# Kernel tuning notes

Hardware: AMD Instinct MI355X
Metric: run time of the kernel (lower is better)

Reference implementation:

```python
import jax, jax.numpy as jnp
import numpy as np

V = 32000   # shared src/trg vocab size
E = 128     # EMB_DIM
H = 256     # HID_DIM
B = 32      # batch
S = 64      # src len
T = 64      # trg len


def setup_inputs() -> dict:
    key = jax.random.key(0)
    ks = jax.random.split(key, 16)
    s = 0.05
    n = lambda k, shape: jax.random.normal(k, shape, dtype=jnp.float32) * s
    return {
        "src": jax.random.randint(ks[0], (B, S), 0, V),
        "trg": jax.random.randint(ks[1], (B, T), 0, V),
        "enc_emb": n(ks[2], (V, E)),
        "enc_Wih": n(ks[3], (4 * H, E)),
        "enc_Whh": n(ks[4], (4 * H, H)),
        "enc_b": n(ks[5], (4 * H,)),   # b_ih + b_hh fused
        "dec_emb": n(ks[6], (V, E)),
        "dec_Wih": n(ks[7], (4 * H, E)),
        "dec_Whh": n(ks[8], (4 * H, H)),
        "dec_b": n(ks[9], (4 * H,)),
        "fc_W": n(ks[10], (V, H)),
        "fc_b": n(ks[11], (V,)),
    }


def _lstm_scan(x_seq, h0, c0, Wih, Whh, b):
    # x_seq: [T, B, E]; PyTorch gate order: i, f, g, o
    def step(carry, x):
        h, c = carry
        gates = x @ Wih.T + h @ Whh.T + b          # [B, 4H]
        i, f, g, o = jnp.split(gates, 4, axis=-1)
        c = jax.nn.sigmoid(f) * c + jax.nn.sigmoid(i) * jnp.tanh(g)
        h = jax.nn.sigmoid(o) * jnp.tanh(c)
        return (h, c), h
    (h, c), hs = jax.lax.scan(step, (h0, c0), x_seq)
    return h, c, hs


def reference(src, trg, enc_emb, enc_Wih, enc_Whh, enc_b,
              dec_emb, dec_Wih, dec_Whh, dec_b, fc_W, fc_b):
    dtype = enc_emb.dtype
    h0 = jnp.zeros((B, H), dtype)
    c0 = jnp.zeros((B, H), dtype)

    # Encoder: embed src, run LSTM, keep final (hidden, cell)
    src_e = enc_emb[src].transpose(1, 0, 2)        # [S, B, E]
    h, c, _ = _lstm_scan(src_e, h0, c0, enc_Wih, enc_Whh, enc_b)

    # Decoder with teacher_forcing_ratio=1.0: input at step t is trg[:, t-1]
    dec_in = dec_emb[trg[:, :-1]].transpose(1, 0, 2)   # [T-1, B, E]
    _, _, hs = _lstm_scan(dec_in, h, c, dec_Wih, dec_Whh, dec_b)  # [T-1, B, H]

    logits = hs @ fc_W.T + fc_b                    # [T-1, B, V]
    # outputs[:, 0, :] stays zero as in the torch code
    outputs = jnp.concatenate(
        [jnp.zeros((1, B, fc_W.shape[0]), dtype), logits], axis=0)
    return outputs.transpose(1, 0, 2)              # [B, T, V]
```

## Files before the change

kernel.cpp:

```cpp
#include <hip/hip_runtime.h>


typedef _Float16 f16x2 __attribute__((ext_vector_type(2)));
typedef short short8 __attribute__((ext_vector_type(8)));
typedef float f32x4 __attribute__((ext_vector_type(4)));
typedef unsigned long long u64;

#define DEV __device__ __forceinline__

static constexpr int Vv = 32000, Ee = 128, Hh = 256, Bb = 32, Ss = 64, Tt = 64;
static constexpr int G4 = 4 * Hh;
static constexpr int MR = (Tt - 1) * Bb;
static constexpr size_t OUT_BT = (size_t)Tt * Vv;

static constexpr size_t OFF_ENCPRE = 0;
static constexpr size_t OFF_DECPRE = OFF_ENCPRE + (size_t)Ss * Bb * G4 * 4;
static constexpr size_t OFF_WQE    = OFF_DECPRE + (size_t)(Tt - 1) * Bb * G4 * 4;
static constexpr size_t OFF_WQD    = OFF_WQE + (size_t)G4 * Hh * 2;
static constexpr size_t OFF_WPE    = OFF_WQD + (size_t)G4 * Hh * 2;
static constexpr size_t OFF_WPD    = OFF_WPE + (size_t)G4 * Ee * 4;
static constexpr size_t OFF_HW     = OFF_WPD + (size_t)G4 * Ee * 4;

DEV float sigm(float x) { return 1.0f / (1.0f + expf(-x)); }

DEV unsigned short f2bf(float x) {
  unsigned u = __float_as_uint(x);
  u = u + 0x7fffu + ((u >> 16) & 1u);
  return (unsigned short)(u >> 16);
}

DEV float dot2(unsigned wu, unsigned hu, float acc) {
  union { unsigned u; f16x2 v; } a, b;
  a.u = wu; b.u = hu;
#if __has_builtin(__builtin_amdgcn_fdot2)
  return __builtin_amdgcn_fdot2(a.v, b.v, acc, false);
#else
  return acc + (float)a.v.x * (float)b.v.x + (float)a.v.y * (float)b.v.y;
#endif
}

__global__ __launch_bounds__(256) void k_pack_whh(const float* __restrict__ src,
                                                  _Float16* __restrict__ dst) {
  int tid = blockIdx.x * 256 + threadIdx.x;
  if (tid >= G4 * Hh) return;
  int r = tid >> 8, k = tid & 255;
  dst[((size_t)(k >> 3) * G4 + r) * 8 + (k & 7)] = (_Float16)src[tid];
}

__global__ __launch_bounds__(256) void k_pack_wih(const float* __restrict__ src,
                                                  float* __restrict__ dst) {
  int tid = blockIdx.x * 256 + threadIdx.x;
  if (tid >= G4 * Ee) return;
  int g = tid >> 7, e = tid & 127;
  dst[((size_t)(e >> 2) * G4 + g) * 4 + (e & 3)] = src[tid];
}

__global__ __launch_bounds__(256) void k_init(u64* __restrict__ w) {
  w[blockIdx.x * 256 + threadIdx.x] = 0ull;
}

__global__ __launch_bounds__(1024) void k_pre(
    const int* __restrict__ src, const int* __restrict__ trg,
    const float* __restrict__ enc_emb, const float* __restrict__ dec_emb,
    const float* __restrict__ WpE, const float* __restrict__ WpD,
    const float* __restrict__ enc_b, const float* __restrict__ dec_b,
    float* __restrict__ enc_pre, float* __restrict__ dec_pre) {
  int blk = blockIdx.x;
  int step = blk >> 2;
  int b0 = (blk & 3) * 8;
  bool enc = step < Ss;
  int ts = enc ? step : step - Ss;
  const int*   tok  = enc ? src : trg;
  const float* emb  = enc ? enc_emb : dec_emb;
  const float* Wp   = enc ? WpE : WpD;
  const float* bias = enc ? enc_b : dec_b;
  float* pre = enc ? (enc_pre + ((size_t)step * Bb + b0) * G4)
                   : (dec_pre + ((size_t)(step - Ss) * Bb + b0) * G4);

  __shared__ __align__(16) float xs[8][128];
  int tid = threadIdx.x;
  {
    int bl = tid >> 7, e = tid & 127;
    int token = tok[(b0 + bl) * 64 + ts];
    xs[bl][e] = emb[(size_t)token * Ee + e];
  }
  __syncthreads();

  int g = tid;
  float acc[8];
  float bv = bias[g];
#pragma unroll
  for (int bb = 0; bb < 8; ++bb) acc[bb] = bv;

  const f32x4* w4 = (const f32x4*)Wp;
  const f32x4(*x4)[32] = (const f32x4(*)[32])xs;
#pragma unroll 4
  for (int e4 = 0; e4 < 32; ++e4) {
    f32x4 w = w4[(size_t)e4 * G4 + g];
#pragma unroll
    for (int bb = 0; bb < 8; ++bb) {
      f32x4 xv = x4[bb][e4];
      acc[bb] += w.x * xv.x + w.y * xv.y + w.z * xv.z + w.w * xv.w;
    }
  }
#pragma unroll
  for (int bb = 0; bb < 8; ++bb) pre[(size_t)bb * G4 + g] = acc[bb];
}

__global__ __launch_bounds__(256, 1) void k_lstm2(
    const float* __restrict__ enc_pre, const float* __restrict__ dec_pre,
    const _Float16* __restrict__ WqE, const _Float16* __restrict__ WqD,
    u64* __restrict__ hword, unsigned short* __restrict__ hsb) {
  const int bid = blockIdx.x;
  const int j = bid >> 5, b = bid & 31;
  const int t = threadIdx.x;
  const int wv = t >> 6, l = t & 63;
  const int c_loc = l & 31, khalf = l >> 5;
  const int r_loc = wv * 32 + c_loc;
  const int row = wv * 256 + j * 32 + c_loc;

  __shared__ uint4 wlds[2][32][128];
  __shared__ unsigned hbits[128];
  __shared__ float gbuf[4][32];
  __shared__ float hstash[32];

  {
    const uint4* gE = (const uint4*)WqE + row;
    const uint4* gD = (const uint4*)WqD + row;
#pragma unroll 4
    for (int kk = 0; kk < 32; ++kk) wlds[0][kk][r_loc] = gE[(size_t)kk * G4];
#pragma unroll 4
    for (int kk = 0; kk < 32; ++kk) wlds[1][kk][r_loc] = gD[(size_t)kk * G4];
  }
  float c = 0.0f;
  __syncthreads();

  for (int step = 0; step < 127; ++step) {
    const bool enc = step < Ss;
    const float* pre = (enc ? enc_pre + (size_t)step * (Bb * G4)
                            : dec_pre + (size_t)(step - Ss) * (Bb * G4)) +
                       (size_t)b * G4;
    float pv = pre[row];

    if (t < 128) {
      if (step == 0) {
        hbits[t] = 0u;
      } else {
        u64* wp = hword + ((size_t)(step & 1) * 32 + b) * 128 + t;
        u64 v;
        do {
          v = __hip_atomic_load(wp, __ATOMIC_RELAXED, __HIP_MEMORY_SCOPE_AGENT);
        } while ((unsigned)(v >> 32) != (unsigned)step);
        hbits[t] = (unsigned)v;
      }
    }
    __syncthreads();

    const uint4* wl = &wlds[enc ? 0 : 1][khalf * 16][0];
    const uint4* hv4 = (const uint4*)hbits;
    float a0 = 0.f, a1 = 0.f, a2 = 0.f, a3 = 0.f;
#pragma unroll
    for (int k8 = 0; k8 < 16; ++k8) {
      uint4 w8 = wl[k8 * 128 + r_loc];
      uint4 h8 = hv4[khalf * 16 + k8];
      a0 = dot2(w8.x, h8.x, a0);
      a1 = dot2(w8.y, h8.y, a1);
      a2 = dot2(w8.z, h8.z, a2);
      a3 = dot2(w8.w, h8.w, a3);
    }
    float acc = (a0 + a1) + (a2 + a3);
    acc += __shfl_xor(acc, 32, 64);
    if (l < 32) gbuf[wv][c_loc] = acc + pv;
    __syncthreads();

    if (t < 32) {
      float gi = gbuf[0][t], gf = gbuf[1][t], gg = gbuf[2][t], go = gbuf[3][t];
      c = sigm(gf) * c + sigm(gi) * tanhf(gg);
      float hn = sigm(go) * tanhf(c);
      hstash[t] = hn;
      if (!enc)
        hsb[((size_t)(step - Ss) * Bb + b) * Hh + j * 32 + t] = f2bf(hn);
      if ((t & 1) == 0) {
        union { _Float16 f; unsigned short u; } u0, u1;
        u0.f = (_Float16)hn;
        u1.f = (_Float16)hstash[t + 1];
        u64 wd = ((u64)(unsigned)(step + 1) << 32) |
                 ((unsigned)u1.u << 16) | (unsigned)u0.u;
        __hip_atomic_store(
            hword + ((size_t)((step + 1) & 1) * 32 + b) * 128 + j * 16 + (t >> 1),
            wd, __ATOMIC_RELAXED, __HIP_MEMORY_SCOPE_AGENT);
      }
    }
  }
}

__global__ __launch_bounds__(256) void k_zero0(float* __restrict__ out) {
  int v = blockIdx.x * 256 + threadIdx.x;
  out[(size_t)blockIdx.y * OUT_BT + v] = 0.0f;
}

__global__ __launch_bounds__(256) void k_fc(const unsigned short* __restrict__ hsb,
                                            const float* __restrict__ fcW,
                                            const float* __restrict__ fcb,
                                            float* __restrict__ out) {
  constexpr int LDB = 264;
  __shared__ __align__(16) unsigned short As[64 * LDB];
  __shared__ __align__(16) unsigned short Bs[64 * LDB];
  int n0 = blockIdx.x * 64;
  int tid = threadIdx.x;
  int lane = tid & 63, wave = tid >> 6;
  int l15 = lane & 15, q = lane >> 4;
  int msub = (wave & 1) * 32, nsub = (wave >> 1) * 32;

#pragma unroll
  for (int r = 0; r < 8; ++r) {
    int vecid = tid + 256 * r;
    int i = vecid >> 5;
    int kk = (vecid & 31) * 8;
    const float* pb = fcW + (size_t)(n0 + i) * Hh + kk;
    short8 vb;
#pragma unroll
    for (int e = 0; e < 8; ++e) vb[e] = (short)f2bf(pb[e]);
    *(short8*)&Bs[i * LDB + kk] = vb;
  }
  float bv0 = fcb[n0 + nsub + l15];
  float bv1 = fcb[n0 + nsub + 16 + l15];

  for (int mt = 0; mt < 32; ++mt) {
    int m0 = mt * 64;
    __syncthreads();
#pragma unroll
    for (int r = 0; r < 8; ++r) {
      int vecid = tid + 256 * r;
      int i = vecid >> 5;
      int kk = (vecid & 31) * 8;
      int gm = m0 + i;
      short8 va = {};
      if (gm < MR) va = *(const short8*)&hsb[(size_t)gm * Hh + kk];
      *(short8*)&As[i * LDB + kk] = va;
    }
    __syncthreads();

    f32x4 acc[2][2] = {};
#pragma unroll
    for (int ks = 0; ks < 8; ++ks) {
      int koff = ks * 32 + q * 8;
      short8 a0 = *(const short8*)&As[(msub + l15) * LDB + koff];
      short8 a1 = *(const short8*)&As[(msub + 16 + l15) * LDB + koff];
      short8 b0 = *(const short8*)&Bs[(nsub + l15) * LDB + koff];
      short8 b1 = *(const short8*)&Bs[(nsub + 16 + l15) * LDB + koff];
      acc[0][0] = __builtin_amdgcn_mfma_f32_16x16x32_bf16(a0, b0, acc[0][0], 0, 0, 0);
      acc[0][1] = __builtin_amdgcn_mfma_f32_16x16x32_bf16(a0, b1, acc[0][1], 0, 0, 0);
      acc[1][0] = __builtin_amdgcn_mfma_f32_16x16x32_bf16(a1, b0, acc[1][0], 0, 0, 0);
      acc[1][1] = __builtin_amdgcn_mfma_f32_16x16x32_bf16(a1, b1, acc[1][1], 0, 0, 0);
    }
#pragma unroll
    for (int ni = 0; ni < 2; ++ni) {
      int gn = n0 + nsub + ni * 16 + l15;
      float bv = ni ? bv1 : bv0;
#pragma unroll
      for (int mi = 0; mi < 2; ++mi) {
#pragma unroll
        for (int r = 0; r < 4; ++r) {
          int gm = m0 + msub + mi * 16 + q * 4 + r;
          if (gm < MR) {
            int tt = gm >> 5, bb = gm & 31;
            out[(size_t)bb * OUT_BT + (size_t)(tt + 1) * Vv + gn] = acc[mi][ni][r] + bv;
          }
        }
      }
    }
  }
}

extern "C" void kernel_launch(void* const* d_in, const int* in_sizes, int n_in,
                              void* d_out, int out_size, void* d_ws, size_t ws_size,
                              hipStream_t stream) {
  const int*   src     = (const int*)d_in[0];
  const int*   trg     = (const int*)d_in[1];
  const float* enc_emb = (const float*)d_in[2];
  const float* enc_Wih = (const float*)d_in[3];
  const float* enc_Whh = (const float*)d_in[4];
  const float* enc_b   = (const float*)d_in[5];
  const float* dec_emb = (const float*)d_in[6];
  const float* dec_Wih = (const float*)d_in[7];
  const float* dec_Whh = (const float*)d_in[8];
  const float* dec_b   = (const float*)d_in[9];
  const float* fc_W    = (const float*)d_in[10];
  const float* fc_b    = (const float*)d_in[11];
  float* out = (float*)d_out;

  char* ob = (char*)d_out;
  float*     enc_pre = (float*)(ob + OFF_ENCPRE);
  float*     dec_pre = (float*)(ob + OFF_DECPRE);
  _Float16*  WqE     = (_Float16*)(ob + OFF_WQE);
  _Float16*  WqD     = (_Float16*)(ob + OFF_WQD);
  float*     WpE     = (float*)(ob + OFF_WPE);
  float*     WpD     = (float*)(ob + OFF_WPD);
  u64*       hword   = (u64*)(ob + OFF_HW);
  unsigned short* hsb = (unsigned short*)d_ws;

  k_init<<<32, 256, 0, stream>>>(hword);
  k_pack_whh<<<1024, 256, 0, stream>>>(enc_Whh, WqE);
  k_pack_whh<<<1024, 256, 0, stream>>>(dec_Whh, WqD);
  k_pack_wih<<<512, 256, 0, stream>>>(enc_Wih, WpE);
  k_pack_wih<<<512, 256, 0, stream>>>(dec_Wih, WpD);
  k_pre<<<508, 1024, 0, stream>>>(src, trg, enc_emb, dec_emb, WpE, WpD,
                                  enc_b, dec_b, enc_pre, dec_pre);
  k_lstm2<<<256, 256, 0, stream>>>(enc_pre, dec_pre, WqE, WqD, hword, hsb);
  k_zero0<<<dim3(125, 32), 256, 0, stream>>>(out);
  k_fc<<<dim3(500), 256, 0, stream>>>(hsb, fc_W, fc_b, out);
}
```

Measured before the change: 641.3 us.

## Merge prep kernels, poll one sentinel per slice, fold zero-fill into FC

New measurement: 637.3 us. Within noise of the previous version (-0.6%).

```diff
diff --git a/kernel.cpp b/kernel.cpp
--- a/kernel.cpp
+++ b/kernel.cpp
@@ -2,6 +2,7 @@
 
 
 typedef _Float16 f16x2 __attribute__((ext_vector_type(2)));
+typedef _Float16 f16x8 __attribute__((ext_vector_type(8)));
 typedef short short8 __attribute__((ext_vector_type(8)));
 typedef float f32x4 __attribute__((ext_vector_type(4)));
 typedef unsigned long long u64;
@@ -39,24 +40,36 @@
 #endif
 }
 
-__global__ __launch_bounds__(256) void k_pack_whh(const float* __restrict__ src,
-                                                  _Float16* __restrict__ dst) {
-  int tid = blockIdx.x * 256 + threadIdx.x;
-  if (tid >= G4 * Hh) return;
-  int r = tid >> 8, k = tid & 255;
-  dst[((size_t)(k >> 3) * G4 + r) * 8 + (k & 7)] = (_Float16)src[tid];
-}
-
-__global__ __launch_bounds__(256) void k_pack_wih(const float* __restrict__ src,
-                                                  float* __restrict__ dst) {
-  int tid = blockIdx.x * 256 + threadIdx.x;
-  if (tid >= G4 * Ee) return;
-  int g = tid >> 7, e = tid & 127;
-  dst[((size_t)(e >> 2) * G4 + g) * 4 + (e & 3)] = src[tid];
-}
-
-__global__ __launch_bounds__(256) void k_init(u64* __restrict__ w) {
-  w[blockIdx.x * 256 + threadIdx.x] = 0ull;
+__global__ __launch_bounds__(256) void k_prep(
+    const float* __restrict__ WhhE_s, const float* __restrict__ WhhD_s,
+    const float* __restrict__ WihE_s, const float* __restrict__ WihD_s,
+    _Float16* __restrict__ WqE, _Float16* __restrict__ WqD,
+    float* __restrict__ WpE, float* __restrict__ WpD,
+    u64* __restrict__ hword) {
+  int blk = blockIdx.x, t = threadIdx.x;
+  if (blk < 32) { hword[blk * 256 + t] = 0ull; return; }
+  blk -= 32;
+  if (blk < 256) {
+    const float* src = (blk < 128) ? WhhE_s : WhhD_s;
+    _Float16*    dst = (blk < 128) ? WqE : WqD;
+    int u = (blk & 127) * 256 + t;
+    int k8 = u >> 10, r = u & 1023;
+    const float* sp = src + r * Hh + k8 * 8;
+    f16x8 v;
+#pragma unroll
+    for (int e = 0; e < 8; ++e) v[e] = (_Float16)sp[e];
+    *(f16x8*)&dst[(size_t)u * 8] = v;
+    return;
+  }
+  blk -= 256;
+  {
+    const float* src = (blk < 128) ? WihE_s : WihD_s;
+    float*       dst = (blk < 128) ? WpE : WpD;
+    int u = (blk & 127) * 256 + t;
+    int e4 = u >> 10, g = u & 1023;
+    f32x4 v = *(const f32x4*)(src + g * Ee + e4 * 4);
+    *(f32x4*)&dst[(size_t)u * 4] = v;
+  }
 }
 
 __global__ __launch_bounds__(1024) void k_pre(
@@ -107,7 +120,7 @@
   for (int bb = 0; bb < 8; ++bb) pre[(size_t)bb * G4 + g] = acc[bb];
 }
 
-__global__ __launch_bounds__(256, 1) void k_lstm2(
+__global__ __launch_bounds__(256, 1) void k_lstm3(
     const float* __restrict__ enc_pre, const float* __restrict__ dec_pre,
     const _Float16* __restrict__ WqE, const _Float16* __restrict__ WqD,
     u64* __restrict__ hword, unsigned short* __restrict__ hsb) {
@@ -146,12 +159,25 @@
       if (step == 0) {
         hbits[t] = 0u;
       } else {
-        u64* wp = hword + ((size_t)(step & 1) * 32 + b) * 128 + t;
-        u64 v;
-        do {
-          v = __hip_atomic_load(wp, __ATOMIC_RELAXED, __HIP_MEMORY_SCOPE_AGENT);
-        } while ((unsigned)(v >> 32) != (unsigned)step);
-        hbits[t] = (unsigned)v;
+        const int p = t >> 4;
+        if (p != j) {
+          u64* base = hword + ((size_t)(step & 1) * 32 + b) * 128;
+          u64* sp = base + p * 16 + 15;
+          u64 s;
+          do {
+            s = __hip_atomic_load(sp, __ATOMIC_RELAXED, __HIP_MEMORY_SCOPE_AGENT);
+          } while ((unsigned)(s >> 32) != (unsigned)step);
+          u64 v;
+          if ((t & 15) == 15) {
+            v = s;
+          } else {
+            u64* wp = base + t;
+            do {
+              v = __hip_atomic_load(wp, __ATOMIC_RELAXED, __HIP_MEMORY_SCOPE_AGENT);
+            } while ((unsigned)(v >> 32) != (unsigned)step);
+          }
+          hbits[t] = (unsigned)v;
+        }
       }
     }
     __syncthreads();
@@ -189,14 +215,10 @@
         __hip_atomic_store(
             hword + ((size_t)((step + 1) & 1) * 32 + b) * 128 + j * 16 + (t >> 1),
             wd, __ATOMIC_RELAXED, __HIP_MEMORY_SCOPE_AGENT);
+        hbits[j * 16 + (t >> 1)] = (unsigned)wd;
       }
     }
   }
-}
-
-__global__ __launch_bounds__(256) void k_zero0(float* __restrict__ out) {
-  int v = blockIdx.x * 256 + threadIdx.x;
-  out[(size_t)blockIdx.y * OUT_BT + v] = 0.0f;
 }
 
 __global__ __launch_bounds__(256) void k_fc(const unsigned short* __restrict__ hsb,
@@ -211,6 +233,15 @@
   int lane = tid & 63, wave = tid >> 6;
   int l15 = lane & 15, q = lane >> 4;
   int msub = (wave & 1) * 32, nsub = (wave >> 1) * 32;
+
+  {
+    int idx = tid * 8;
+    int zb = idx >> 6, off = idx & 63;
+    float* zp = out + (size_t)zb * OUT_BT + n0 + off;
+    f32x4 z = {};
+    *(f32x4*)zp = z;
+    *(f32x4*)(zp + 4) = z;
+  }
 
 #pragma unroll
   for (int r = 0; r < 8; ++r) {
@@ -300,14 +331,10 @@
   u64*       hword   = (u64*)(ob + OFF_HW);
   unsigned short* hsb = (unsigned short*)d_ws;
 
-  k_init<<<32, 256, 0, stream>>>(hword);
-  k_pack_whh<<<1024, 256, 0, stream>>>(enc_Whh, WqE);
-  k_pack_whh<<<1024, 256, 0, stream>>>(dec_Whh, WqD);
-  k_pack_wih<<<512, 256, 0, stream>>>(enc_Wih, WpE);
-  k_pack_wih<<<512, 256, 0, stream>>>(dec_Wih, WpD);
+  k_prep<<<544, 256, 0, stream>>>(enc_Whh, dec_Whh, enc_Wih, dec_Wih,
+                                  WqE, WqD, WpE, WpD, hword);
   k_pre<<<508, 1024, 0, stream>>>(src, trg, enc_emb, dec_emb, WpE, WpD,
                                   enc_b, dec_b, enc_pre, dec_pre);
-  k_lstm2<<<256, 256, 0, stream>>>(enc_pre, dec_pre, WqE, WqD, hword, hsb);
-  k_zero0<<<dim3(125, 32), 256, 0, stream>>>(out);
+  k_lstm3<<<256, 256, 0, stream>>>(enc_pre, dec_pre, WqE, WqD, hword, hsb);
   k_fc<<<dim3(500), 256, 0, stream>>>(hsb, fc_W, fc_b, out);
 }
```
